# Kernel tuning notes

Hardware: AMD Instinct MI355X
Metric: run time of the kernel (lower is better)

The kernel has to match this reference:

```python
import jax, jax.numpy as jnp
import numpy as np

N_NODES = 50000
N_GRAPHS = 512


def _gcn_layer(x, src, dst, W, b):
    # DGL GraphConv, norm='both', allow_zero_in_degree=True
    n = x.shape[0]
    ones = jnp.ones(src.shape[0], x.dtype)
    deg_out = jnp.zeros(n, x.dtype).at[src].add(ones)
    deg_in = jnp.zeros(n, x.dtype).at[dst].add(ones)
    norm_out = jax.lax.rsqrt(jnp.maximum(deg_out, 1.0))
    norm_in = jax.lax.rsqrt(jnp.maximum(deg_in, 1.0))
    h = x * norm_out[:, None]
    agg = jax.ops.segment_sum(h[src], dst, num_segments=n)  # SpMM
    return (agg * norm_in[:, None]) @ W + b


def setup_inputs() -> dict:
    key = jax.random.key(0)
    ks = jax.random.split(key, 16)
    E = 800000
    inp = {
        'nid': jax.random.randint(ks[0], (N_NODES,), 0, 100000),
        'z': jax.random.randint(ks[1], (N_NODES,), 0, 1000),
        'src': jax.random.randint(ks[2], (E,), 0, N_NODES),
        'dst': jax.random.randint(ks[3], (E,), 0, N_NODES),
        'graph_id': jnp.sort(jax.random.randint(ks[4], (N_NODES,), 0, N_GRAPHS)),
        'init_embed': jax.random.normal(ks[5], (100000, 64), jnp.float32) * 0.1,
        'z_table': jax.random.normal(ks[6], (1000, 64), jnp.float32) * 0.1,
        'W0': jax.random.normal(ks[7], (128, 128), jnp.float32) * 0.1,
        'b0': jnp.zeros((128,), jnp.float32),
        'W1': jax.random.normal(ks[8], (128, 128), jnp.float32) * 0.1,
        'b1': jnp.zeros((128,), jnp.float32),
        'W2': jax.random.normal(ks[9], (128, 128), jnp.float32) * 0.1,
        'b2': jnp.zeros((128,), jnp.float32),
        'lin1_W': jax.random.normal(ks[10], (128, 128), jnp.float32) * 0.1,
        'lin1_b': jnp.zeros((128,), jnp.float32),
        'lin2_W': jax.random.normal(ks[11], (128, 200), jnp.float32) * 0.1,
        'lin2_b': jnp.zeros((200,), jnp.float32),
    }
    return inp


def reference(nid, z, src, dst, graph_id, init_embed, z_table, W0, b0, W1, b1, W2, b2, lin1_W, lin1_b, lin2_W, lin2_b):
    # node features: entity embedding lookup + structural label embedding, concat
    x = jnp.concatenate([init_embed[nid], z_table[z]], axis=1)  # [N, 128]
    # layers[:-1] with relu (dropout is identity in eval mode)
    x = jax.nn.relu(_gcn_layer(x, src, dst, W0, b0))
    x = jax.nn.relu(_gcn_layer(x, src, dst, W1, b1))
    x = _gcn_layer(x, src, dst, W2, b2)
    # SumPooling over subgraphs in the batch
    g = jax.ops.segment_sum(x, graph_id, num_segments=N_GRAPHS)  # [G, 128]
    h = jax.nn.relu(g @ lin1_W + lin1_b)
    return h @ lin2_W + lin2_b  # [G, num_rel]
```

## Files before the change

kernel.cpp:

```cpp
#include <hip/hip_runtime.h>
#include <hip/hip_bf16.h>


#define FEAT 128
#define NG 512
#define CH 128
#define NPMAX 12544
#define LDW 136

typedef __attribute__((ext_vector_type(8))) short bf16x8;
typedef __attribute__((ext_vector_type(4))) float f32x4;

__device__ __forceinline__ float bf2f(unsigned short u) {
    union { unsigned int i; float f; } v; v.i = ((unsigned int)u) << 16; return v.f;
}
__device__ __forceinline__ unsigned short f2bf(float f) {
    unsigned int u = __float_as_uint(f);
    return (unsigned short)((u + 0x7FFFu + ((u >> 16) & 1u)) >> 16);
}
__device__ __forceinline__ float lo16(unsigned u) { return __uint_as_float(u << 16); }
__device__ __forceinline__ float hi16(unsigned u) { return __uint_as_float(u & 0xFFFF0000u); }

__global__ __launch_bounds__(256) void k_hist(
        const int* __restrict__ src, const int* __restrict__ dst,
        unsigned* __restrict__ partial_out, unsigned* __restrict__ partial_in,
        int E, int NP, int Ec) {
    __shared__ unsigned h[NPMAX];
    int tid = threadIdx.x;
    int b = blockIdx.x;
    int c = b & (CH - 1);
    const int* __restrict__ arr = (b < CH) ? src : dst;
    unsigned* __restrict__ outp = ((b < CH) ? partial_out : partial_in) + (size_t)c * NP;
    for (int i = tid; i < NP; i += 256) h[i] = 0;
    __syncthreads();
    int e0 = c * Ec, e1 = min(E, e0 + Ec);
    for (int e = e0 + tid; e < e1; e += 256) {
        int v = arr[e];
        atomicAdd(&h[v >> 2], 1u << ((v & 3) * 8));
    }
    __syncthreads();
    for (int i = tid; i < NP; i += 256) outp[i] = h[i];
}

__global__ void k_merge(unsigned* __restrict__ partial_out, unsigned* __restrict__ partial_in,
                        int* __restrict__ cnt_in, float* __restrict__ norm_out,
                        float* __restrict__ norm_in, int N, int NP) {
    int w = blockIdx.x * blockDim.x + threadIdx.x;
    if (w >= NP) return;
    unsigned run_in = 0, run_out = 0;
    for (int c = 0; c < CH; c++) {
        size_t idx = (size_t)c * NP + w;
        unsigned v = partial_in[idx];
        partial_in[idx] = run_in;
        run_in += v;
        run_out += partial_out[idx];
    }
    #pragma unroll
    for (int j = 0; j < 4; j++) {
        int node = w * 4 + j;
        if (node < N) {
            unsigned di = (run_in  >> (j * 8)) & 255u;
            unsigned dd = (run_out >> (j * 8)) & 255u;
            cnt_in[node]   = (int)di;
            norm_in[node]  = rsqrtf(fmaxf((float)di, 1.0f));
            norm_out[node] = rsqrtf(fmaxf((float)dd, 1.0f));
        }
    }
}

__global__ void k_scan_local(const int* __restrict__ cnt, int* __restrict__ excl,
                             int* __restrict__ bsum, int N) {
    __shared__ int s[256];
    int x = threadIdx.x;
    int i = blockIdx.x * 256 + x;
    int v = (i < N) ? cnt[i] : 0;
    s[x] = v;
    __syncthreads();
    for (int off = 1; off < 256; off <<= 1) {
        int t = (x >= off) ? s[x - off] : 0;
        __syncthreads();
        s[x] += t;
        __syncthreads();
    }
    if (i < N) excl[i] = s[x] - v;
    if (x == 255) bsum[blockIdx.x] = s[255];
}

__global__ void k_scan_bsum_prep(int* __restrict__ bsum, int* __restrict__ boff, int nb,
                                 const float* __restrict__ W0, const float* __restrict__ W1,
                                 unsigned short* __restrict__ WF0, unsigned short* __restrict__ WF1) {
    if (blockIdx.x == 0) {
        __shared__ int s[256];
        int x = threadIdx.x;
        int v = (x < nb) ? bsum[x] : 0;
        s[x] = v;
        __syncthreads();
        for (int off = 1; off < 256; off <<= 1) {
            int t = (x >= off) ? s[x - off] : 0;
            __syncthreads();
            s[x] += t;
            __syncthreads();
        }
        if (x < nb) boff[x] = s[x] - v;
    } else {
        int t = ((int)blockIdx.x - 1) * 256 + threadIdx.x;
        const float* __restrict__ W = (t < 16384) ? W0 : W1;
        unsigned short* __restrict__ WF = (t < 16384) ? WF0 : WF1;
        int tt = t & 16383;
        int f = tt >> 9, l = (tt >> 3) & 63, e = tt & 7;
        int n = (f >> 2) * 16 + (l & 15);
        int k = (f & 3) * 32 + (l >> 4) * 8 + e;
        WF[tt] = f2bf(W[k * 128 + n]);
    }
}

__global__ void k_add_off(int* __restrict__ row_start, const int* __restrict__ boff,
                          float* __restrict__ g, int N) {
    int i = blockIdx.x * blockDim.x + threadIdx.x;
    int stride = gridDim.x * blockDim.x;
    if (i < N) row_start[i] += boff[i >> 8];
    for (int j = i; j < NG * FEAT; j += stride) g[j] = 0.f;
}

__global__ __launch_bounds__(256) void k_fill_bx(
        const int* __restrict__ src, const int* __restrict__ dst,
        const int* __restrict__ row_start, const unsigned* __restrict__ partial_in,
        unsigned short* __restrict__ csr,
        const int* __restrict__ nid, const int* __restrict__ z,
        const float* __restrict__ emb, const float* __restrict__ zt,
        const float* __restrict__ nout, unsigned short* __restrict__ x,
        int N, int E, int NP, int Ec) {
    if ((int)blockIdx.x < CH) {
        __shared__ unsigned cur[NPMAX];
        int tid = threadIdx.x;
        int c = blockIdx.x;
        const unsigned* __restrict__ pre = partial_in + (size_t)c * NP;
        for (int i = tid; i < NP; i += 256) cur[i] = pre[i];
        __syncthreads();
        int e0 = c * Ec, e1 = min(E, e0 + Ec);
        for (int e = e0 + tid; e < e1; e += 256) {
            int d = dst[e], s = src[e];
            int sh = (d & 3) * 8;
            unsigned t = atomicAdd(&cur[d >> 2], 1u << sh);
            int off = (int)((t >> sh) & 255u);
            csr[row_start[d] + off] = (unsigned short)s;
        }
    } else {
        int tid = ((int)blockIdx.x - CH) * 256 + threadIdx.x;
        int i = tid >> 5, q = tid & 31;
        if (i < N) {
            float4 v;
            if (q < 16) v = ((const float4*)emb)[(size_t)nid[i] * 16 + q];
            else        v = ((const float4*)zt)[(size_t)z[i] * 16 + (q - 16)];
            float w = nout[i];
            ushort4 u;
            u.x = f2bf(v.x * w); u.y = f2bf(v.y * w);
            u.z = f2bf(v.z * w); u.w = f2bf(v.w * w);
            ((ushort4*)x)[(size_t)i * 32 + q] = u;
        }
    }
}

#define ACC8(u)                                                                  \
    a0 += lo16(u.x); a1 += hi16(u.x); a2 += lo16(u.y); a3 += hi16(u.y);          \
    a4 += lo16(u.z); a5 += hi16(u.z); a6 += lo16(u.w); a7 += hi16(u.w);

#define GATHER_LOOP                                                              \
    {                                                                            \
        int base = row_start[node];                                              \
        int n = cnt_in[node];                                                    \
        const uint4* xp = (const uint4*)x;                   \
        for (int j0 = 0; j0 < n; j0 += 16) {                                     \
            int rem = n - j0;                                                    \
            int m = rem < 16 ? rem : 16;                                         \
            int e = (int)csr[base + j0 + (ql < m ? ql : 0)];                     \
            int j = 0;                                                           \
            for (; j + 8 <= m; j += 8) {                                         \
                int s0 = __shfl(e, j + 0, 16), s1 = __shfl(e, j + 1, 16);        \
                int s2 = __shfl(e, j + 2, 16), s3 = __shfl(e, j + 3, 16);        \
                int s4 = __shfl(e, j + 4, 16), s5 = __shfl(e, j + 5, 16);        \
                int s6 = __shfl(e, j + 6, 16), s7 = __shfl(e, j + 7, 16);        \
                uint4 u0 = xp[(size_t)s0 * 16 + ql];                             \
                uint4 u1 = xp[(size_t)s1 * 16 + ql];                             \
                uint4 u2 = xp[(size_t)s2 * 16 + ql];                             \
                uint4 u3 = xp[(size_t)s3 * 16 + ql];                             \
                uint4 u4 = xp[(size_t)s4 * 16 + ql];                             \
                uint4 u5 = xp[(size_t)s5 * 16 + ql];                             \
                uint4 u6 = xp[(size_t)s6 * 16 + ql];                             \
                uint4 u7 = xp[(size_t)s7 * 16 + ql];                             \
                ACC8(u0) ACC8(u1) ACC8(u2) ACC8(u3)                              \
                ACC8(u4) ACC8(u5) ACC8(u6) ACC8(u7)                              \
            }                                                                    \
            for (; j + 4 <= m; j += 4) {                                         \
                int s0 = __shfl(e, j + 0, 16), s1 = __shfl(e, j + 1, 16);        \
                int s2 = __shfl(e, j + 2, 16), s3 = __shfl(e, j + 3, 16);        \
                uint4 u0 = xp[(size_t)s0 * 16 + ql];                             \
                uint4 u1 = xp[(size_t)s1 * 16 + ql];                             \
                uint4 u2 = xp[(size_t)s2 * 16 + ql];                             \
                uint4 u3 = xp[(size_t)s3 * 16 + ql];                             \
                ACC8(u0) ACC8(u1) ACC8(u2) ACC8(u3)                              \
            }                                                                    \
            for (; j < m; j++) {                                                 \
                int s = __shfl(e, j, 16);                                        \
                uint4 u = xp[(size_t)s * 16 + ql];                               \
                ACC8(u)                                                          \
            }                                                                    \
        }                                                                        \
    }

__global__ __launch_bounds__(256) void k_gather_gemm(
        const unsigned short* __restrict__ x, const float* __restrict__ nin,
        const unsigned short* __restrict__ csr, const int* __restrict__ row_start,
        const int* __restrict__ cnt_in, const unsigned short* __restrict__ WF,
        const float* __restrict__ bias, const float* __restrict__ nout,
        unsigned short* __restrict__ y, int N) {
    __shared__ unsigned short As[16 * LDW];
    int tid = threadIdx.x;
    int nb = blockIdx.x * 16;
    int ql = tid & 15;
    int nl = tid >> 4;
    int node = nb + nl;

    float a0 = 0.f, a1 = 0.f, a2 = 0.f, a3 = 0.f;
    float a4 = 0.f, a5 = 0.f, a6 = 0.f, a7 = 0.f;
    if (node < N) {
        GATHER_LOOP
        float ni = nin[node];
        a0 *= ni; a1 *= ni; a2 *= ni; a3 *= ni;
        a4 *= ni; a5 *= ni; a6 *= ni; a7 *= ni;
    }
    uint4 o;
    o.x = (unsigned)f2bf(a0) | ((unsigned)f2bf(a1) << 16);
    o.y = (unsigned)f2bf(a2) | ((unsigned)f2bf(a3) << 16);
    o.z = (unsigned)f2bf(a4) | ((unsigned)f2bf(a5) << 16);
    o.w = (unsigned)f2bf(a6) | ((unsigned)f2bf(a7) << 16);
    *(uint4*)(As + nl * LDW + ql * 8) = o;
    __syncthreads();

    int lane = tid & 63;
    int wv = tid >> 6;
    int c = lane & 15, q = lane >> 4;

    const unsigned short* ap = As + c * LDW + q * 8;
    bf16x8 fa0 = *(const bf16x8*)(ap);
    bf16x8 fa1 = *(const bf16x8*)(ap + 32);
    bf16x8 fa2 = *(const bf16x8*)(ap + 64);
    bf16x8 fa3 = *(const bf16x8*)(ap + 96);
    const bf16x8* __restrict__ wf = (const bf16x8*)WF;
    __syncthreads();

    #pragma unroll
    for (int t = 0; t < 2; t++) {
        int nt = wv * 2 + t;
        bf16x8 fb0 = wf[(nt * 4 + 0) * 64 + lane];
        bf16x8 fb1 = wf[(nt * 4 + 1) * 64 + lane];
        bf16x8 fb2 = wf[(nt * 4 + 2) * 64 + lane];
        bf16x8 fb3 = wf[(nt * 4 + 3) * 64 + lane];
        float bb = bias[nt * 16 + c];
        f32x4 acc = {bb, bb, bb, bb};
        acc = __builtin_amdgcn_mfma_f32_16x16x32_bf16(fa0, fb0, acc, 0, 0, 0);
        acc = __builtin_amdgcn_mfma_f32_16x16x32_bf16(fa1, fb1, acc, 0, 0, 0);
        acc = __builtin_amdgcn_mfma_f32_16x16x32_bf16(fa2, fb2, acc, 0, 0, 0);
        acc = __builtin_amdgcn_mfma_f32_16x16x32_bf16(fa3, fb3, acc, 0, 0, 0);
        #pragma unroll
        for (int rr = 0; rr < 4; rr++) {
            int row = q * 4 + rr;
            float s = nout[min(nb + row, N - 1)];
            As[row * LDW + nt * 16 + c] = f2bf(fmaxf(acc[rr], 0.f) * s);
        }
    }
    __syncthreads();

    {
        int row = tid >> 4, seg = tid & 15;
        int nd = nb + row;
        if (nd < N) {
            const ushort4* p = (const ushort4*)(As + row * LDW + seg * 8);
            ushort4* d = (ushort4*)(y + (size_t)nd * 128 + seg * 8);
            d[0] = p[0]; d[1] = p[1];
        }
    }
}

__global__ __launch_bounds__(256) void k_gather_pool(
        const unsigned short* __restrict__ x, const float* __restrict__ nin,
        const unsigned short* __restrict__ csr, const int* __restrict__ row_start,
        const int* __restrict__ cnt_in, const int* __restrict__ gid,
        float* __restrict__ g, int N) {
    __shared__ __align__(16) float gl[16][132];
    __shared__ int slots[16];
    int tid = threadIdx.x;
    int nb = blockIdx.x * 16;
    int ql = tid & 15;
    int nl = tid >> 4;
    int node = nb + nl;

    float a0 = 0.f, a1 = 0.f, a2 = 0.f, a3 = 0.f;
    float a4 = 0.f, a5 = 0.f, a6 = 0.f, a7 = 0.f;
    int slot = -1;
    if (node < N) {
        GATHER_LOOP
        float ni = nin[node];
        a0 *= ni; a1 *= ni; a2 *= ni; a3 *= ni;
        a4 *= ni; a5 *= ni; a6 *= ni; a7 *= ni;
        slot = gid[node];
    }
    float4* row = (float4*)&gl[nl][ql * 8];
    row[0] = make_float4(a0, a1, a2, a3);
    row[1] = make_float4(a4, a5, a6, a7);
    if (ql == 0) slots[nl] = slot;
    __syncthreads();

    int h = tid >> 7;
    int j = tid & 127;
    int prev = -1;
    float acc = 0.f;
    #pragma unroll
    for (int i = h * 8; i < h * 8 + 8; i++) {
        int s = slots[i];
        if (s != prev) {
            if (prev >= 0) atomicAdd(&g[(size_t)prev * FEAT + j], acc);
            acc = 0.f;
            prev = s;
        }
        acc += gl[i][j];
    }
    if (prev >= 0) atomicAdd(&g[(size_t)prev * FEAT + j], acc);
}

__global__ __launch_bounds__(256) void k_head(
        const float* __restrict__ g, const int* __restrict__ gid,
        const float* __restrict__ W2, const float* __restrict__ b2,
        const float* __restrict__ l1W, const float* __restrict__ l1b,
        const float* __restrict__ l2W, const float* __restrict__ l2b,
        float* __restrict__ out, int N) {
    __shared__ float gs[128];
    __shared__ float ys[128];
    __shared__ float hs[128];
    int gi = blockIdx.x, tid = threadIdx.x;

    int lo = 0, hi = N;
    while (lo < hi) { int m = (lo + hi) >> 1; if (gid[m] < gi) lo = m + 1; else hi = m; }
    int s0 = lo;
    lo = 0; hi = N;
    while (lo < hi) { int m = (lo + hi) >> 1; if (gid[m] < gi + 1) lo = m + 1; else hi = m; }
    float cnt = (float)(lo - s0);

    if (tid < 128) gs[tid] = g[(size_t)gi * FEAT + tid];
    __syncthreads();
    if (tid < 128) {
        float a = cnt * b2[tid];
        for (int k = 0; k < 128; k++) a += gs[k] * W2[(size_t)k * 128 + tid];
        ys[tid] = a;
    }
    __syncthreads();
    if (tid < 128) {
        float a = l1b[tid];
        for (int k = 0; k < 128; k++) a += ys[k] * l1W[(size_t)k * 128 + tid];
        hs[tid] = fmaxf(a, 0.f);
    }
    __syncthreads();
    if (tid < 200) {
        float a = l2b[tid];
        for (int k = 0; k < 128; k++) a += hs[k] * l2W[(size_t)k * 200 + tid];
        out[(size_t)gi * 200 + tid] = a;
    }
}

extern "C" void kernel_launch(void* const* d_in, const int* in_sizes, int n_in,
                              void* d_out, int out_size, void* d_ws, size_t ws_size,
                              hipStream_t stream) {
    const int*   nid = (const int*)d_in[0];
    const int*   z   = (const int*)d_in[1];
    const int*   src = (const int*)d_in[2];
    const int*   dst = (const int*)d_in[3];
    const int*   gid = (const int*)d_in[4];
    const float* emb = (const float*)d_in[5];
    const float* zt  = (const float*)d_in[6];
    const float* W0  = (const float*)d_in[7];
    const float* b0  = (const float*)d_in[8];
    const float* W1  = (const float*)d_in[9];
    const float* b1  = (const float*)d_in[10];
    const float* W2  = (const float*)d_in[11];
    const float* b2  = (const float*)d_in[12];
    const float* l1W = (const float*)d_in[13];
    const float* l1b = (const float*)d_in[14];
    const float* l2W = (const float*)d_in[15];
    const float* l2b = (const float*)d_in[16];
    float* out = (float*)d_out;

    const int N = in_sizes[0];
    const int E = in_sizes[2];
    const int NB = (N + 255) / 256;
    const int NP = (N + 3) / 4;
    const int Ec = (E + CH - 1) / CH;

    size_t NA = (size_t)((N + 63) & ~63);
    float* norm_out = (float*)d_ws;
    float* norm_in  = norm_out + NA;
    float* g        = norm_in + NA;
    unsigned short* xA  = (unsigned short*)(g + (size_t)NG * FEAT);
    unsigned short* xB  = xA + (size_t)N * FEAT;
    unsigned short* WF0 = xB + (size_t)N * FEAT;
    unsigned short* WF1 = WF0 + 128 * 128;
    int* cnt_in    = (int*)(WF1 + 128 * 128);
    int* row_start = cnt_in + NA;
    int* bsum      = row_start + NA;
    int* boff      = bsum + 256;
    unsigned* partial_out = (unsigned*)(boff + 256);
    unsigned* partial_in  = partial_out + (size_t)CH * NP;
    unsigned short* csr = (unsigned short*)(partial_in + (size_t)CH * NP);

    k_hist<<<2 * CH, 256, 0, stream>>>(src, dst, partial_out, partial_in, E, NP, Ec);
    k_merge<<<(NP + 255) / 256, 256, 0, stream>>>(partial_out, partial_in, cnt_in,
                                                  norm_out, norm_in, N, NP);
    k_scan_local<<<NB, 256, 0, stream>>>(cnt_in, row_start, bsum, N);
    k_scan_bsum_prep<<<1 + 128, 256, 0, stream>>>(bsum, boff, NB, W0, W1, WF0, WF1);
    k_add_off<<<NB, 256, 0, stream>>>(row_start, boff, g, N);
    int XB = (N * 32 + 255) / 256;
    k_fill_bx<<<CH + XB, 256, 0, stream>>>(src, dst, row_start, partial_in, csr,
                                           nid, z, emb, zt, norm_out, xA, N, E, NP, Ec);

    int gg_blocks = (N + 15) / 16;

    k_gather_gemm<<<gg_blocks, 256, 0, stream>>>(xA, norm_in, csr, row_start, cnt_in,
                                                 WF0, b0, norm_out, xB, N);
    k_gather_gemm<<<gg_blocks, 256, 0, stream>>>(xB, norm_in, csr, row_start, cnt_in,
                                                 WF1, b1, norm_out, xA, N);
    k_gather_pool<<<gg_blocks, 256, 0, stream>>>(xA, norm_in, csr, row_start, cnt_in,
                                                 gid, g, N);

    k_head<<<NG, 256, 0, stream>>>(g, gid, W2, b2, l1W, l1b, l2W, l2b, out, N);
}
```

Baseline: 277.8 us.

## Replace LDS packed-histogram CSR build with global atomic degree counts and cursors

The degree count and CSR fill move from per-chunk 8-bit packed LDS histograms, with a 128-chunk merge/prefix pass, to plain global int atomics on per-node counters and a per-node cursor. This removes the k_merge pass, the large 12.5K-entry LDS allocations, and the partial histogram traffic, at the cost of contended global atomics on 800K edges. CSR order within a row becomes nondeterministic, which can change float summation order. It also adds a minimum occupancy hint of 8 blocks to the gather kernels.

After: 328.5 us. +18.2%, slower.

```diff
diff --git a/kernel.cpp b/kernel.cpp
--- a/kernel.cpp
+++ b/kernel.cpp
@@ -4,16 +4,12 @@
 
 #define FEAT 128
 #define NG 512
-#define CH 128
-#define NPMAX 12544
 #define LDW 136
+#define FB 256
 
 typedef __attribute__((ext_vector_type(8))) short bf16x8;
 typedef __attribute__((ext_vector_type(4))) float f32x4;
 
-__device__ __forceinline__ float bf2f(unsigned short u) {
-    union { unsigned int i; float f; } v; v.i = ((unsigned int)u) << 16; return v.f;
-}
 __device__ __forceinline__ unsigned short f2bf(float f) {
     unsigned int u = __float_as_uint(f);
     return (unsigned short)((u + 0x7FFFu + ((u >> 16) & 1u)) >> 16);
@@ -21,59 +17,37 @@
 __device__ __forceinline__ float lo16(unsigned u) { return __uint_as_float(u << 16); }
 __device__ __forceinline__ float hi16(unsigned u) { return __uint_as_float(u & 0xFFFF0000u); }
 
-__global__ __launch_bounds__(256) void k_hist(
+__global__ __launch_bounds__(256) void k_zero(
+        int* __restrict__ ci, int* __restrict__ co, float* __restrict__ g, int N) {
+    int i = blockIdx.x * 256 + threadIdx.x;
+    int s = gridDim.x * 256;
+    for (int j = i; j < N; j += s) { ci[j] = 0; co[j] = 0; }
+    for (int j = i; j < NG * FEAT; j += s) g[j] = 0.f;
+}
+
+__global__ __launch_bounds__(256) void k_deg(
         const int* __restrict__ src, const int* __restrict__ dst,
-        unsigned* __restrict__ partial_out, unsigned* __restrict__ partial_in,
-        int E, int NP, int Ec) {
-    __shared__ unsigned h[NPMAX];
-    int tid = threadIdx.x;
-    int b = blockIdx.x;
-    int c = b & (CH - 1);
-    const int* __restrict__ arr = (b < CH) ? src : dst;
-    unsigned* __restrict__ outp = ((b < CH) ? partial_out : partial_in) + (size_t)c * NP;
-    for (int i = tid; i < NP; i += 256) h[i] = 0;
-    __syncthreads();
-    int e0 = c * Ec, e1 = min(E, e0 + Ec);
-    for (int e = e0 + tid; e < e1; e += 256) {
-        int v = arr[e];
-        atomicAdd(&h[v >> 2], 1u << ((v & 3) * 8));
-    }
-    __syncthreads();
-    for (int i = tid; i < NP; i += 256) outp[i] = h[i];
-}
-
-__global__ void k_merge(unsigned* __restrict__ partial_out, unsigned* __restrict__ partial_in,
-                        int* __restrict__ cnt_in, float* __restrict__ norm_out,
-                        float* __restrict__ norm_in, int N, int NP) {
-    int w = blockIdx.x * blockDim.x + threadIdx.x;
-    if (w >= NP) return;
-    unsigned run_in = 0, run_out = 0;
-    for (int c = 0; c < CH; c++) {
-        size_t idx = (size_t)c * NP + w;
-        unsigned v = partial_in[idx];
-        partial_in[idx] = run_in;
-        run_in += v;
-        run_out += partial_out[idx];
-    }
-    #pragma unroll
-    for (int j = 0; j < 4; j++) {
-        int node = w * 4 + j;
-        if (node < N) {
-            unsigned di = (run_in  >> (j * 8)) & 255u;
-            unsigned dd = (run_out >> (j * 8)) & 255u;
-            cnt_in[node]   = (int)di;
-            norm_in[node]  = rsqrtf(fmaxf((float)di, 1.0f));
-            norm_out[node] = rsqrtf(fmaxf((float)dd, 1.0f));
-        }
-    }
-}
-
-__global__ void k_scan_local(const int* __restrict__ cnt, int* __restrict__ excl,
-                             int* __restrict__ bsum, int N) {
+        int* __restrict__ ci, int* __restrict__ co, int E) {
+    int i = blockIdx.x * 256 + threadIdx.x;
+    int s = gridDim.x * 256;
+    for (int e = i; e < E; e += s) {
+        atomicAdd(&ci[dst[e]], 1);
+        atomicAdd(&co[src[e]], 1);
+    }
+}
+
+__global__ void k_scan_local(const int* __restrict__ cnt, const int* __restrict__ cnto,
+                             int* __restrict__ excl, int* __restrict__ bsum,
+                             float* __restrict__ nin, float* __restrict__ nout, int N) {
     __shared__ int s[256];
     int x = threadIdx.x;
     int i = blockIdx.x * 256 + x;
-    int v = (i < N) ? cnt[i] : 0;
+    int v = 0;
+    if (i < N) {
+        v = cnt[i];
+        nin[i]  = rsqrtf(fmaxf((float)v, 1.0f));
+        nout[i] = rsqrtf(fmaxf((float)cnto[i], 1.0f));
+    }
     s[x] = v;
     __syncthreads();
     for (int off = 1; off < 256; off <<= 1) {
@@ -115,38 +89,32 @@
 }
 
 __global__ void k_add_off(int* __restrict__ row_start, const int* __restrict__ boff,
-                          float* __restrict__ g, int N) {
+                          int* __restrict__ cursor, int N) {
     int i = blockIdx.x * blockDim.x + threadIdx.x;
-    int stride = gridDim.x * blockDim.x;
-    if (i < N) row_start[i] += boff[i >> 8];
-    for (int j = i; j < NG * FEAT; j += stride) g[j] = 0.f;
+    if (i < N) {
+        int r = row_start[i] + boff[i >> 8];
+        row_start[i] = r;
+        cursor[i] = r;
+    }
 }
 
 __global__ __launch_bounds__(256) void k_fill_bx(
         const int* __restrict__ src, const int* __restrict__ dst,
-        const int* __restrict__ row_start, const unsigned* __restrict__ partial_in,
-        unsigned short* __restrict__ csr,
+        int* __restrict__ cursor, unsigned short* __restrict__ csr,
         const int* __restrict__ nid, const int* __restrict__ z,
         const float* __restrict__ emb, const float* __restrict__ zt,
         const float* __restrict__ nout, unsigned short* __restrict__ x,
-        int N, int E, int NP, int Ec) {
-    if ((int)blockIdx.x < CH) {
-        __shared__ unsigned cur[NPMAX];
-        int tid = threadIdx.x;
-        int c = blockIdx.x;
-        const unsigned* __restrict__ pre = partial_in + (size_t)c * NP;
-        for (int i = tid; i < NP; i += 256) cur[i] = pre[i];
-        __syncthreads();
-        int e0 = c * Ec, e1 = min(E, e0 + Ec);
-        for (int e = e0 + tid; e < e1; e += 256) {
-            int d = dst[e], s = src[e];
-            int sh = (d & 3) * 8;
-            unsigned t = atomicAdd(&cur[d >> 2], 1u << sh);
-            int off = (int)((t >> sh) & 255u);
-            csr[row_start[d] + off] = (unsigned short)s;
+        int N, int E) {
+    if ((int)blockIdx.x < FB) {
+        int i = blockIdx.x * 256 + threadIdx.x;
+        int s = FB * 256;
+        for (int e = i; e < E; e += s) {
+            int d = dst[e];
+            int slot = atomicAdd(&cursor[d], 1);
+            csr[slot] = (unsigned short)src[e];
         }
     } else {
-        int tid = ((int)blockIdx.x - CH) * 256 + threadIdx.x;
+        int tid = ((int)blockIdx.x - FB) * 256 + threadIdx.x;
         int i = tid >> 5, q = tid & 31;
         if (i < N) {
             float4 v;
@@ -208,7 +176,7 @@
         }                                                                        \
     }
 
-__global__ __launch_bounds__(256) void k_gather_gemm(
+__global__ __launch_bounds__(256, 8) void k_gather_gemm(
         const unsigned short* __restrict__ x, const float* __restrict__ nin,
         const unsigned short* __restrict__ csr, const int* __restrict__ row_start,
         const int* __restrict__ cnt_in, const unsigned short* __restrict__ WF,
@@ -282,7 +250,7 @@
     }
 }
 
-__global__ __launch_bounds__(256) void k_gather_pool(
+__global__ __launch_bounds__(256, 8) void k_gather_pool(
         const unsigned short* __restrict__ x, const float* __restrict__ nin,
         const unsigned short* __restrict__ csr, const int* __restrict__ row_start,
         const int* __restrict__ cnt_in, const int* __restrict__ gid,
@@ -392,8 +360,6 @@
     const int N = in_sizes[0];
     const int E = in_sizes[2];
     const int NB = (N + 255) / 256;
-    const int NP = (N + 3) / 4;
-    const int Ec = (E + CH - 1) / CH;
 
     size_t NA = (size_t)((N + 63) & ~63);
     float* norm_out = (float*)d_ws;
@@ -404,22 +370,22 @@
     unsigned short* WF0 = xB + (size_t)N * FEAT;
     unsigned short* WF1 = WF0 + 128 * 128;
     int* cnt_in    = (int*)(WF1 + 128 * 128);
-    int* row_start = cnt_in + NA;
-    int* bsum      = row_start + NA;
+    int* cnt_out   = cnt_in + NA;
+    int* row_start = cnt_out + NA;
+    int* cursor    = row_start + NA;
+    int* bsum      = cursor + NA;
     int* boff      = bsum + 256;
-    unsigned* partial_out = (unsigned*)(boff + 256);
-    unsigned* partial_in  = partial_out + (size_t)CH * NP;
-    unsigned short* csr = (unsigned short*)(partial_in + (size_t)CH * NP);
-
-    k_hist<<<2 * CH, 256, 0, stream>>>(src, dst, partial_out, partial_in, E, NP, Ec);
-    k_merge<<<(NP + 255) / 256, 256, 0, stream>>>(partial_out, partial_in, cnt_in,
-                                                  norm_out, norm_in, N, NP);
-    k_scan_local<<<NB, 256, 0, stream>>>(cnt_in, row_start, bsum, N);
+    unsigned short* csr = (unsigned short*)(boff + 256);
+
+    k_zero<<<512, 256, 0, stream>>>(cnt_in, cnt_out, g, N);
+    k_deg<<<2048, 256, 0, stream>>>(src, dst, cnt_in, cnt_out, E);
+    k_scan_local<<<NB, 256, 0, stream>>>(cnt_in, cnt_out, row_start, bsum,
+                                         norm_in, norm_out, N);
     k_scan_bsum_prep<<<1 + 128, 256, 0, stream>>>(bsum, boff, NB, W0, W1, WF0, WF1);
-    k_add_off<<<NB, 256, 0, stream>>>(row_start, boff, g, N);
+    k_add_off<<<NB, 256, 0, stream>>>(row_start, boff, cursor, N);
     int XB = (N * 32 + 255) / 256;
-    k_fill_bx<<<CH + XB, 256, 0, stream>>>(src, dst, row_start, partial_in, csr,
-                                           nid, z, emb, zt, norm_out, xA, N, E, NP, Ec);
+    k_fill_bx<<<FB + XB, 256, 0, stream>>>(src, dst, cursor, csr,
+                                           nid, z, emb, zt, norm_out, xA, N, E);
 
     int gg_blocks = (N + 15) / 16;
 
```
